# Kernel optimization log

Measured on AMD Instinct MI355X. Metric: run time of the kernel, lower is better.

Reference implementation:

```python
import jax, jax.numpy as jnp
import numpy as np

BN_EPS = 1e-5
GRID = 8  # 8x8 region grid
AU_NUM = 12


def conv2d(x, w, b, stride=1, pad=0):
    # x: [B,C,H,W], w: [O,I,kh,kw]
    y = jax.lax.conv_general_dilated(
        x, w, (stride, stride), [(pad, pad), (pad, pad)],
        dimension_numbers=("NCHW", "OIHW", "NCHW"))
    return y + b[None, :, None, None]


def bn_eval(x, gamma, beta, mean, var):
    inv = jax.lax.rsqrt(var + BN_EPS)
    return (x - mean[None, :, None, None]) * (gamma * inv)[None, :, None, None] + beta[None, :, None, None]


def region_layer(x, gamma, beta, mean, var, cw, cb):
    # x: [B,C,H,W]; per-network params indexed by k = i*j + j (faithful to source)
    B, C, H, W = x.shape
    ph, pw = H // GRID, W // GRID
    # -> [64, B, C, ph, pw]
    p = x.reshape(B, C, GRID, ph, GRID, pw).transpose(2, 4, 0, 1, 3, 5).reshape(GRID * GRID, B, C, ph, pw)
    ii = jnp.arange(GRID)[:, None]
    jj = jnp.arange(GRID)[None, :]
    idx = (ii * jj + jj).reshape(-1)  # replicates self.networks[i*j+j]

    def per_patch(xp, g, bt, m, v, w, b):
        xn = bn_eval(xp, g, bt, m, v)
        xr = jax.nn.relu(xn)
        return conv2d(xr, w, b, stride=1, pad=1) + xp

    out = jax.vmap(per_patch)(p, gamma[idx], beta[idx], mean[idx], var[idx], cw[idx], cb[idx])
    # [64,B,C,ph,pw] -> [B,C,H,W]
    return out.reshape(GRID, GRID, B, C, ph, pw).transpose(2, 3, 0, 4, 1, 5).reshape(B, C, H, W)


def maxpool2(x):
    return jax.lax.reduce_window(x, -jnp.inf, jax.lax.max, (1, 1, 2, 2), (1, 1, 2, 2), "VALID")


def setup_inputs() -> dict:
    key = jax.random.key(0)
    ks = iter(jax.random.split(key, 40))
    n = lambda shape, s=0.05: jax.random.normal(next(ks), shape, jnp.float32) * s
    d = {}
    d["x"] = jax.random.normal(next(ks), (32, 3, 170, 170), jnp.float32)
    d["conv1_w"] = n((32, 3, 11, 11)); d["conv1_b"] = n((32,))
    NG = GRID * GRID
    d["rl_gamma"] = 1.0 + n((NG, 32)); d["rl_beta"] = n((NG, 32))
    d["rl_mean"] = n((NG, 32)); d["rl_var"] = 0.5 + jax.random.uniform(next(ks), (NG, 32), jnp.float32)
    d["rl_cw"] = n((NG, 32, 32, 3, 3)); d["rl_cb"] = n((NG, 32))
    d["bn_gamma"] = 1.0 + n((32,)); d["bn_beta"] = n((32,))
    d["bn_mean"] = n((32,)); d["bn_var"] = 0.5 + jax.random.uniform(next(ks), (32,), jnp.float32)
    d["conv2_w"] = n((16, 32, 8, 8)); d["conv2_b"] = n((16,))
    d["conv3_w"] = n((16, 16, 8, 8)); d["conv3_b"] = n((16,))
    d["conv4_w"] = n((16, 16, 6, 6)); d["conv4_b"] = n((16,))
    d["conv5_w"] = n((16, 16, 5, 5)); d["conv5_b"] = n((16,))
    d["fc1_w"] = n((4096, 16 * 27 * 27), 0.01); d["fc1_b"] = n((4096,))
    d["fc2_w"] = n((2048, 4096), 0.01); d["fc2_b"] = n((2048,))
    d["fc3_w"] = n((AU_NUM * 2, 2048), 0.01); d["fc3_b"] = n((AU_NUM * 2,))
    return d


def reference(x, conv1_w, conv1_b, rl_gamma, rl_beta, rl_mean, rl_var, rl_cw, rl_cb,
              bn_gamma, bn_beta, bn_mean, bn_var, conv2_w, conv2_b, conv3_w, conv3_b,
              conv4_w, conv4_b, conv5_w, conv5_b, fc1_w, fc1_b, fc2_w, fc2_b, fc3_w, fc3_b):
    B = x.shape[0]
    h = conv2d(x, conv1_w, conv1_b)                       # [B,32,160,160]
    h = region_layer(h, rl_gamma, rl_beta, rl_mean, rl_var, rl_cw, rl_cb)
    h = jax.nn.relu(h)
    h = maxpool2(h)                                       # [B,32,80,80]
    h = bn_eval(h, bn_gamma, bn_beta, bn_mean, bn_var)
    h = jax.nn.relu(conv2d(h, conv2_w, conv2_b))          # [B,16,73,73]
    h = jax.nn.relu(conv2d(h, conv3_w, conv3_b))          # [B,16,66,66]
    h = jax.nn.relu(conv2d(h, conv4_w, conv4_b, stride=2))  # [B,16,31,31]
    h = jax.nn.relu(conv2d(h, conv5_w, conv5_b))          # [B,16,27,27]
    h = h.reshape(B, -1)
    h = jax.nn.relu(h @ fc1_w.T + fc1_b)
    h = jax.nn.relu(h @ fc2_w.T + fc2_b)  # dropout = identity (eval)
    h = h @ fc3_w.T + fc3_b
    h = h.reshape(B, 2, AU_NUM)
    return jax.nn.log_softmax(h, axis=1)
```

## Files before the change

### kernel.cpp

```cpp
#include <hip/hip_runtime.h>
#include <hip/hip_bf16.h>

typedef __hip_bfloat16 bf16;
typedef __attribute__((ext_vector_type(8))) short short8;
typedef __attribute__((ext_vector_type(4))) float f32x4;
typedef __attribute__((ext_vector_type(16))) float f32x16;

__device__ __forceinline__ float b2f(const bf16 v){ return __bfloat162float(v); }
__device__ __forceinline__ float ld(const float* p, long i){ return p[i]; }
__device__ __forceinline__ float ld(const bf16*  p, long i){ return b2f(p[i]); }

__device__ __forceinline__ unsigned f2bf_u(float f){
    union { float f; unsigned u; } a; a.f = f;
    unsigned r = a.u + 0x7FFFu + ((a.u >> 16) & 1u);
    return r >> 16;
}

__device__ __forceinline__ short8 pack8(const float* v){
    union { __hip_bfloat162 h[4]; short8 s; } r;
    #pragma unroll
    for (int i=0;i<4;i++)
        r.h[i] = __float22bfloat162_rn(float2{v[2*i], v[2*i+1]});
    return r.s;
}

__device__ __forceinline__ uint2 pack4(const float* v){
    union { __hip_bfloat162 h[2]; uint2 u; } r;
    r.h[0] = __float22bfloat162_rn(float2{v[0], v[1]});
    r.h[1] = __float22bfloat162_rn(float2{v[2], v[3]});
    return r.u;
}

__device__ __forceinline__ void unp8(uint4 u, float* v){
    union { unsigned x; float f; } a;
    a.x = u.x<<16; v[0]=a.f; a.x = u.x&0xffff0000u; v[1]=a.f;
    a.x = u.y<<16; v[2]=a.f; a.x = u.y&0xffff0000u; v[3]=a.f;
    a.x = u.z<<16; v[4]=a.f; a.x = u.z&0xffff0000u; v[5]=a.f;
    a.x = u.w<<16; v[6]=a.f; a.x = u.w&0xffff0000u; v[7]=a.f;
}

__device__ __forceinline__ void unp4(uint2 u, float* v){
    union { unsigned x; float f; } a;
    a.x = u.x<<16; v[0]=a.f; a.x = u.x&0xffff0000u; v[1]=a.f;
    a.x = u.y<<16; v[2]=a.f; a.x = u.y&0xffff0000u; v[3]=a.f;
}

#define GLD_LDS16(g, l) __builtin_amdgcn_global_load_lds( \
    (const __attribute__((address_space(1))) void*)(g), \
    (__attribute__((address_space(3))) void*)(l), 16, 0, 0)

#define OFF_C1W   0
#define OFF_C1B   11616
#define OFF_RLG   11648
#define OFF_RLB   13696
#define OFF_RLM   15744
#define OFF_RLV   17792
#define OFF_RLCW  19840
#define OFF_RLCB  609664
#define OFF_BNG   611712
#define OFF_BNB   611744
#define OFF_BNM   611776
#define OFF_BNV   611808
#define OFF_C2W   611840
#define OFF_C2B   644608
#define OFF_C3W   644624
#define OFF_C3B   661008
#define OFF_C4W   661024
#define OFF_C4B   670240
#define OFF_C5W   670256
#define OFF_C5B   676656
#define OFF_F1B   676672
#define OFF_F2B   680768
#define OFF_F3B   682816
#define P_TOTAL   682840
#define OFF_WB2   P_TOTAL
#define OFF_WB3   (P_TOTAL + 16384)
#define OFF_WC1   (P_TOTAL + 16384 + 8192)
#define P_END     (OFF_WC1 + 8448)

#define SZ_RL  589824
#define SZ_WB2 32768
#define SZ_WB3 16384
#define SZ_WC1 16896

struct CvtArgs { const void* src[23]; int off[23]; const void* cw; const void* w2; const void* w3;
                 const void* x0; int total; };

__device__ __forceinline__ float getv(const void* p, long i, bool isf){
    return isf ? ((const float*)p)[i] : b2f(((const bf16*)p)[i]);
}

__global__ __launch_bounds__(256) void k_cvt(CvtArgs a, int* __restrict__ flag,
                                             float* __restrict__ P)
{
    __shared__ int cnt;
    if (threadIdx.x == 0) cnt = 0;
    __syncthreads();
    {
        const bf16* xb = (const bf16*)a.x0;
        const float v = fabsf(b2f(xb[2*threadIdx.x]));
        if (v >= 1e-6f && v <= 1e6f) atomicAdd(&cnt, 1);
    }
    __syncthreads();
    const bool isf = (cnt < 192);
    if (blockIdx.x == 0 && threadIdx.x == 0) *flag = isf ? 1 : 0;

    const int i1 = a.total;
    const int i2 = i1 + SZ_RL;
    const int i3 = i2 + SZ_WB2;
    const int i4 = i3 + SZ_WB3;
    const int i5 = i4 + SZ_WC1;
    for (int idx = blockIdx.x*256 + threadIdx.x; idx < i5; idx += gridDim.x*256){
        if (idx < i1){
            if (idx >= OFF_RLCW && idx < OFF_RLCB) continue;
            int k = 0;
            #pragma unroll
            for (int j = 1; j < 23; j++) if (idx >= a.off[j]) k = j;
            P[idx] = getv(a.src[k], idx - a.off[k], isf);
        } else if (idx < i2){
            const int d = idx - i1;
            const int net = d / 9216, dn = d % 9216;
            const int tap = dn >> 10, rem = dn & 1023;
            const int half = rem >> 9, lane = (rem >> 3) & 63, j = rem & 7;
            const int co = half*16 + (lane & 15);
            const int ci = ((lane >> 4) << 3) + j;
            const long sidx = (long)((net*32 + co)*32 + ci)*9 + tap;
            ((unsigned short*)(P + OFF_RLCW))[d] = (unsigned short)f2bf_u(getv(a.cw, sidx, isf));
        } else if (idx < i3){
            const int d = idx - i2;
            const int j = d & 7, lane = (d >> 3) & 63, tap = d >> 9;
            const int n = lane & 15, k = ((lane >> 4) << 3) + j;
            const int ci = k, ky = tap >> 3, kx = tap & 7;
            const long sidx = (long)((n*32 + ci)*8 + ky)*8 + kx;
            ((unsigned short*)(P + OFF_WB2))[d] = (unsigned short)f2bf_u(getv(a.w2, sidx, isf));
        } else if (idx < i4){
            const int d = idx - i3;
            const int j = d & 7, lane = (d >> 3) & 63, pair = d >> 9;
            const int n = lane & 15, k = ((lane >> 4) << 3) + j;
            const int tsel = k >> 4, ci = k & 15;
            const int ky = pair >> 2, kx = ((pair & 3) << 1) + tsel;
            const long sidx = (long)((n*16 + ci)*8 + ky)*8 + kx;
            ((unsigned short*)(P + OFF_WB3))[d] = (unsigned short)f2bf_u(getv(a.w3, sidx, isf));
        } else {
            const int d = idx - i4;
            const int ky = d / 1536, rem = d % 1536;
            const int ch = rem >> 9, rem2 = rem & 511;
            const int lane = rem2 >> 3, j = rem2 & 7;
            const int co = lane & 31, h5 = lane >> 5;
            const int kx = ch*4 + h5*2 + (j >> 2), ci = j & 3;
            float v = 0.f;
            if (ci < 3 && kx < 11)
                v = getv(a.src[0], (long)((co*3 + ci)*11 + ky)*11 + kx, isf);
            ((unsigned short*)(P + OFF_WC1))[d] = (unsigned short)f2bf_u(v);
        }
    }
}

__global__ __launch_bounds__(256,3) void k_conv1M(const void* __restrict__ x,
        const int* __restrict__ flag, const float* __restrict__ P, unsigned short* __restrict__ out)
{
    __shared__ unsigned short xs[18*44*4];
    __shared__ unsigned short wsm[SZ_WC1];
    const int t = threadIdx.x;
    const int y0 = blockIdx.x*8, x0 = blockIdx.y*32, b = blockIdx.z;
    { const uint4* src = (const uint4*)(P + OFF_WC1);
      uint4* dst = (uint4*)wsm;
      for (int e=t; e<2112; e+=256) dst[e] = src[e]; }
    const bool isf = (*flag) != 0;
    for (int e=t; e<792; e+=256){
        const int r = e/44, c = e%44;
        const long base = ((long)(b*3)*170 + (y0+r))*170 + min(x0+c, 169);
        float v0, v1, v2;
        if (isf){
            const float* xf = (const float*)x;
            v0 = xf[base]; v1 = xf[base+28900]; v2 = xf[base+57800];
        } else {
            const bf16* xf = (const bf16*)x;
            v0 = b2f(xf[base]); v1 = b2f(xf[base+28900]); v2 = b2f(xf[base+57800]);
        }
        uint2 u;
        u.x = f2bf_u(v0) | (f2bf_u(v1) << 16);
        u.y = f2bf_u(v2);
        *(uint2*)&xs[(r*44+c)*4] = u;
    }
    __syncthreads();
    const int wave = t>>6, lane = t&63;
    const int n = lane & 31, h5 = lane >> 5;
    const int r0 = wave*2;
    f32x16 acc0 = {0.f}, acc1 = {0.f};
    #pragma unroll
    for (int e=0;e<16;e++){ acc0[e]=0.f; acc1[e]=0.f; }
    #pragma unroll 1
    for (int ky=0; ky<11; ky++){
        #pragma unroll
        for (int ch=0; ch<3; ch++){
            const short8 aw = *(const short8*)&wsm[((ky*3+ch)*64 + lane)*8];
            const int kx0 = ch*4 + h5*2;
            const int a0 = ((r0+ky)*44 + n + kx0)*4;
            const int a1 = ((r0+1+ky)*44 + n + kx0)*4;
            union { uint2 u2[2]; short8 s; } ub0, ub1;
            ub0.u2[0] = *(const uint2*)&xs[a0];
            ub0.u2[1] = *(const uint2*)&xs[a0+4];
            ub1.u2[0] = *(const uint2*)&xs[a1];
            ub1.u2[1] = *(const uint2*)&xs[a1+4];
            acc0 = __builtin_amdgcn_mfma_f32_32x32x16_bf16(aw, ub0.s, acc0, 0,0,0);
            acc1 = __builtin_amdgcn_mfma_f32_32x32x16_bf16(aw, ub1.s, acc1, 0,0,0);
        }
    }
    unsigned short* opb = out + ((long)b*25600 + (long)(y0+r0)*160 + x0 + n)*32;
    #pragma unroll
    for (int g=0; g<4; g++){
        const int co0 = 8*g + 4*h5;
        const f32x4 bv = *(const f32x4*)&P[OFF_C1B + co0];
        float s0[4], s1[4];
        #pragma unroll
        for (int r=0;r<4;r++){ s0[r] = acc0[4*g+r] + bv[r]; s1[r] = acc1[4*g+r] + bv[r]; }
        *(uint2*)(opb + co0) = pack4(s0);
        *(uint2*)(opb + 160*32 + co0) = pack4(s1);
    }
}

__global__ __launch_bounds__(256,2) void k_regionM(const unsigned short* __restrict__ in,
        const float* __restrict__ P, unsigned short* __restrict__ pooled)
{
    __shared__ unsigned short s_in[484*32];
    __shared__ unsigned short wsm[9216];
    __shared__ float sc[32], sh[32];
    const int t = threadIdx.x;
    const int b = blockIdx.x & 31, kk = blockIdx.x >> 5;
    const int gi = kk >> 3, gj = kk & 7;
    const int net = gj*(gi+1);
    const long pbase = ((long)b*25600 + (long)(gi*20)*160 + gj*20)*32;
    if (t < 32){
        const float inv = rsqrtf(P[OFF_RLV+net*32+t]+1e-5f)*P[OFF_RLG+net*32+t];
        sc[t] = inv; sh[t] = P[OFF_RLB+net*32+t] - P[OFF_RLM+net*32+t]*inv;
    }
    { const uint4* src = (const uint4*)((const unsigned short*)(P+OFF_RLCW) + (size_t)net*9216);
      uint4* dst = (uint4*)wsm;
      for (int e=t; e<1152; e+=256) dst[e] = src[e]; }
    __syncthreads();
    for (int e=t; e<1936; e+=256){
        const int o = e & 3, p = e >> 2;
        const int pr = p/22, pc = p%22;
        short8 pk = {0,0,0,0,0,0,0,0};
        if (pr>0 && pr<21 && pc>0 && pc<21){
            const long a = pbase + ((long)(pr-1)*160 + (pc-1))*32 + o*8;
            const uint4 u = *(const uint4*)&in[a];
            float v[8];
            unp8(u, v);
            #pragma unroll
            for (int j=0;j<8;j++){
                const int ci = o*8 + j;
                v[j] = fmaxf(fmaf(v[j], sc[ci], sh[ci]), 0.f);
            }
            pk = pack8(v);
        }
        *(short8*)&s_in[p*32 + o*8] = pk;
    }
    __syncthreads();
    const int wave = t>>6, lane = t&63;
    const int q = lane>>4, n = lane&15;
    const int dr = n>>2, dc = n&3;
    const int nt = (wave==0) ? 7 : 6;
    int trs[7], tcs[7];
    #pragma unroll
    for (int i=0;i<7;i++){ const int tt = 4*i + wave; trs[i] = tt/5; tcs[i] = tt - 5*(tt/5); }
    f32x4 acc[7][2];
    {   float bias_v[2][4];
        #pragma unroll
        for (int h=0;h<2;h++)
            #pragma unroll
            for (int r=0;r<4;r++) bias_v[h][r] = P[OFF_RLCB + net*32 + h*16 + q*4 + r];
        #pragma unroll
        for (int i=0;i<7;i++)
            #pragma unroll
            for (int h=0;h<2;h++)
                acc[i][h] = (f32x4){bias_v[h][0], bias_v[h][1], bias_v[h][2], bias_v[h][3]};
    }
    #pragma unroll 1
    for (int tap=0; tap<9; tap++){
        const short8 a0 = *(const short8*)&wsm[(tap*2+0)*512 + lane*8];
        const short8 a1 = *(const short8*)&wsm[(tap*2+1)*512 + lane*8];
        const int ky = tap/3, kx = tap - 3*(tap/3);
        #pragma unroll
        for (int i=0;i<7;i++){
            if (i < nt){
                const int srow = trs[i]*4 + dr + ky, scol = tcs[i]*4 + dc + kx;
                const short8 bx = *(const short8*)&s_in[(srow*22 + scol)*32 + q*8];
                acc[i][0] = __builtin_amdgcn_mfma_f32_16x16x32_bf16(a0, bx, acc[i][0], 0,0,0);
                acc[i][1] = __builtin_amdgcn_mfma_f32_16x16x32_bf16(a1, bx, acc[i][1], 0,0,0);
            }
        }
    }
    float bnsc[2][4], bnsh[2][4];
    #pragma unroll
    for (int h=0;h<2;h++)
        #pragma unroll
        for (int r=0;r<4;r++){
            const int co = h*16 + q*4 + r;
            const float inv = rsqrtf(P[OFF_BNV+co]+1e-5f)*P[OFF_BNG+co];
            bnsc[h][r] = inv; bnsh[h][r] = P[OFF_BNB+co] - P[OFF_BNM+co]*inv;
        }
    const bool wr = ((n & 5) == 0);
    #pragma unroll
    for (int i=0;i<7;i++){
        if (i < nt){
            const int prow = trs[i]*4 + dr, pcol = tcs[i]*4 + dc;
            const long ra = pbase + ((long)prow*160 + pcol)*32;
            const long pa0 = ((long)b*6400 + (long)(gi*10 + trs[i]*2 + (dr>>1))*80
                              + gj*10 + tcs[i]*2 + (dc>>1))*32;
            #pragma unroll
            for (int h=0;h<2;h++){
                const uint2 ru = *(const uint2*)&in[ra + h*16 + q*4];
                float res[4];
                unp4(ru, res);
                float pv[4];
                #pragma unroll
                for (int r=0;r<4;r++){
                    float v = acc[i][h][r] + res[r];
                    v = fmaxf(v, 0.f);
                    v = fmaxf(v, __shfl_xor(v, 1, 64));
                    v = fmaxf(v, __shfl_xor(v, 4, 64));
                    pv[r] = fmaf(v, bnsc[h][r], bnsh[h][r]);
                }
                if (wr) *(uint2*)&pooled[pa0 + h*16 + q*4] = pack4(pv);
            }
        }
    }
}

template<int CIN, int HIN, int WIN, int HOUT, int WOUT, bool NHWC_OUT>
__global__ __launch_bounds__(256) void k_convM(const unsigned short* __restrict__ in,
        const unsigned short* __restrict__ WB, const float* __restrict__ bias,
        void* __restrict__ outv)
{
    constexpr int PP = 23;
    constexpr bool C32 = (CIN == 32);
    __shared__ unsigned short xs[PP*PP*CIN];
    __shared__ unsigned short ws[C32 ? 16*64*8 : 32*64*8];
    const int t = threadIdx.x;
    const int col0 = blockIdx.x*16, row0 = blockIdx.y*16, b = blockIdx.z;
    for (int e = t; e < PP*PP*(CIN/8); e += 256){
        const int o = e % (CIN/8), pix = e / (CIN/8);
        int rr = row0 + pix/PP; if (rr > HIN-1) rr = HIN-1;
        int cc = col0 + pix%PP; if (cc > WIN-1) cc = WIN-1;
        const uint4 v = *(const uint4*)&in[((long)b*HIN*WIN + (long)rr*WIN + cc)*CIN + o*8];
        *(uint4*)&xs[pix*CIN + o*8] = v;
    }
    const int wave = t>>6, lane = t&63;
    const int quad = lane>>4, n16 = lane&15;
    const float bv = bias[n16];
    f32x4 acc[4];
    #pragma unroll
    for (int mt=0;mt<4;mt++) acc[mt] = (f32x4){bv,bv,bv,bv};
    if constexpr (C32){
        for (int ch=0; ch<4; ch++){
            __syncthreads();
            const unsigned* src = (const unsigned*)WB + ch*4096;
            for (int e=t; e<4096; e+=256) ((unsigned*)ws)[e] = src[e];
            __syncthreads();
            #pragma unroll 1
            for (int tap=0; tap<16; tap++){
                const int tg = ch*16+tap, ky = tg>>3, kx = tg&7;
                const short8 bw = *(const short8*)&ws[(tap*64+lane)*8];
                #pragma unroll
                for (int mt=0; mt<4; mt++){
                    const int pr = wave*4+mt+ky, pc = n16+kx;
                    const short8 av = *(const short8*)&xs[(pr*PP+pc)*32 + quad*8];
                    acc[mt] = __builtin_amdgcn_mfma_f32_16x16x32_bf16(av, bw, acc[mt], 0,0,0);
                }
            }
        }
    } else {
        for (int e=t; e<8192; e+=256) ((unsigned*)ws)[e] = ((const unsigned*)WB)[e];
        __syncthreads();
        #pragma unroll 1
        for (int pair=0; pair<32; pair++){
            const int ky = pair>>2, kx0 = (pair&3)*2;
            const short8 bw = *(const short8*)&ws[(pair*64+lane)*8];
            #pragma unroll
            for (int mt=0; mt<4; mt++){
                const int pr = wave*4+mt+ky, pc = n16 + kx0 + (quad>>1);
                const short8 av = *(const short8*)&xs[(pr*PP+pc)*16 + (quad&1)*8];
                acc[mt] = __builtin_amdgcn_mfma_f32_16x16x32_bf16(av, bw, acc[mt], 0,0,0);
            }
        }
    }
    #pragma unroll
    for (int mt=0; mt<4; mt++){
        const int orow = row0 + wave*4 + mt;
        if (orow >= HOUT) continue;
        const int ocol = col0 + quad*4;
        #pragma unroll
        for (int r=0;r<4;r++){
            if (ocol + r < WOUT){
                const float v = fmaxf(acc[mt][r], 0.f);
                if constexpr (NHWC_OUT)
                    ((unsigned short*)outv)[((long)b*HOUT*WOUT + (long)orow*WOUT + ocol + r)*16 + n16]
                        = (unsigned short)f2bf_u(v);
                else
                    ((float*)outv)[((long)(b*16 + n16)*HOUT + orow)*WOUT + ocol + r] = v;
            }
        }
    }
}

template<int CIN, int COUT, int KS, int STRIDE, int HIN, int WIN, int HOUT, int WOUT,
         int NG, int OW>
__global__ __launch_bounds__(256,2) void k_convN(const float* __restrict__ in,
        const float* __restrict__ w, const float* __restrict__ bias, float* __restrict__ out)
{
    __shared__ float wl[CIN*KS*KS];
    const int co = blockIdx.y, b = blockIdx.z;
    for (int j=threadIdx.x; j<CIN*KS*KS; j+=blockDim.x) wl[j] = w[co*CIN*KS*KS + j];
    __syncthreads();
    const int i = blockIdx.x*blockDim.x + threadIdx.x;
    if (i >= HOUT*NG) return;
    const int y = i / NG, x0 = (i % NG) * OW;
    float acc[OW];
    const float bv = bias[co];
    #pragma unroll
    for (int j=0;j<OW;j++) acc[j]=bv;
    constexpr int SPAN = STRIDE*(OW-1) + KS;
    for (int ci=0; ci<CIN; ci++){
        #pragma unroll
        for (int ky=0; ky<KS; ky++){
            const float* ip = in + ((long)(b*CIN+ci)*HIN + (STRIDE*y+ky))*WIN + STRIDE*x0;
            float v[SPAN];
            #pragma unroll
            for (int j=0;j<SPAN;j++) v[j]=ip[j];
            const float* wr = &wl[(ci*KS+ky)*KS];
            #pragma unroll
            for (int kx=0;kx<KS;kx++){
                const float wv = wr[kx];
                #pragma unroll
                for (int j=0;j<OW;j++) acc[j] = fmaf(v[STRIDE*j+kx], wv, acc[j]);
            }
        }
    }
    float* op = out + ((long)(b*COUT+co)*HOUT + y)*WOUT + x0;
    #pragma unroll
    for (int j=0;j<OW;j++)
        if (x0 + j < WOUT) op[j] = fmaxf(acc[j], 0.f);
}

__global__ __launch_bounds__(256,2) void k_conv5F(const float* __restrict__ in,
        const float* __restrict__ P, unsigned short* __restrict__ xp, float* __restrict__ y)
{
    __shared__ float wl[16*25];
    const int co = blockIdx.y, b = blockIdx.z;
    const int t = threadIdx.x;
    for (int j=t; j<400; j+=256) wl[j] = P[OFF_C5W + co*400 + j];
    {   const int lin = (b*16 + co)*256 + t;
        y[lin] = P[OFF_F1B + (lin & 4095)];
    }
    if (co == 0 && t < 208){
        unsigned short* pp = xp + (long)b*12288 + 11664 + t*3;
        pp[0] = 0; pp[1] = 0; pp[2] = 0;
    }
    __syncthreads();
    if (t >= 27*7) return;
    const int yy = t / 7, x0 = (t % 7) * 4;
    float acc[4];
    const float bv = P[OFF_C5B + co];
    #pragma unroll
    for (int j=0;j<4;j++) acc[j]=bv;
    for (int ci=0; ci<16; ci++){
        #pragma unroll
        for (int ky=0; ky<5; ky++){
            const float* ip = in + ((long)(b*16+ci)*31 + (yy+ky))*31 + x0;
            float v[8];
            #pragma unroll
            for (int j=0;j<8;j++) v[j]=ip[j];
            const float* wr = &wl[(ci*5+ky)*5];
            #pragma unroll
            for (int kx=0;kx<5;kx++){
                const float wv = wr[kx];
                #pragma unroll
                for (int j=0;j<4;j++) acc[j] = fmaf(v[j+kx], wv, acc[j]);
            }
        }
    }
    unsigned short* op = xp + (long)b*12288 + (co*27 + yy)*27 + x0;
    #pragma unroll
    for (int j=0;j<4;j++)
        if (x0 + j < 27) op[j] = (unsigned short)f2bf_u(fmaxf(acc[j], 0.f));
}

__global__ __launch_bounds__(256) void k_pk(const float* __restrict__ in,
        unsigned short* __restrict__ out, float* __restrict__ y,
        const float* __restrict__ bias, int N, int ny, int rows, int K)
{
    const int i = blockIdx.x*256 + threadIdx.x;
    if (i < ny){ y[i] = bias[i % N]; return; }
    const int d = i - ny;
    const int per = K >> 3;
    if (d >= rows*per) return;
    const int row = d / per, k = (d - row*per)*8;
    float v[8];
    *(f32x4*)&v[0] = *(const f32x4*)&in[(long)row*K + k];
    *(f32x4*)&v[4] = *(const f32x4*)&in[(long)row*K + k + 4];
    #pragma unroll
    for (int j=0;j<8;j++) v[j] = fmaxf(v[j], 0.f);
    *(short8*)&out[(long)row*K + k] = pack8(v);
}

template<typename WT>
__device__ __forceinline__ void fcl_body(const unsigned short* __restrict__ x,
        const WT* __restrict__ w, float* __restrict__ y,
        int Kw, int Khat, int N, int Kc, int Nvalid, unsigned char* lbuf)
{
    constexpr bool WF = __is_same(WT, float);
    const int t = threadIdx.x;
    const int wave = t>>6, lane = t&63;
    const int quad = lane>>4, n16 = lane&15;
    const int og = wave>>1, bh = wave&1;
    const int bx = blockIdx.x;
    const int start = blockIdx.y*Kc;
    int steps = 0;
    {   const int rem = Kw - start;
        const int sa = Kc >> 7;
        if (rem > 0){ steps = (rem + 127) >> 7; if (steps > sa) steps = sa; }
    }
    f32x4 acc = {0.f,0.f,0.f,0.f};
    const unsigned short* xp = x + (long)(bh*16 + n16)*Khat;
    const int row = og*16 + n16;

    auto stage = [&](int s, int bsel){
        const int k0 = start + (s<<7);
        const bool swz = (k0 + 128 <= Kw);
        unsigned char* base = lbuf + bsel*16384;
        if constexpr (WF){
            const int r0 = wave*8;
            #pragma unroll
            for (int c=0;c<4;c++){
                const int rr = r0 + 2*c + (lane>>5);
                const int cs = swz ? ((lane&31) ^ (rr&7)) : (lane&31);
                long koff = (long)k0 + cs*4;
                const float* ga = w + (long)(bx*32 + rr)*Kw + koff;
                if (!swz && (koff + 4 > Kw)) ga = w + (long)(bx*32 + rr)*Kw;
                GLD_LDS16(ga, base + (r0 + 2*c)*512);
            }
        } else {
            const int r0 = wave*8;
            #pragma unroll
            for (int c=0;c<2;c++){
                const int rr = r0 + 4*c + (lane>>4);
                const int cs = swz ? ((lane&15) ^ (rr&7)) : (lane&15);
                long koff = (long)k0 + cs*8;
                const WT* ga = w + (long)(bx*32 + rr)*Kw + koff;
                if (!swz && (koff + 8 > Kw)) ga = w + (long)(bx*32 + rr)*Kw;
                GLD_LDS16(ga, base + (r0 + 4*c)*256);
            }
        }
    };
    auto consume = [&](int s, int bsel){
        const int k0 = start + (s<<7);
        const bool swz = (k0 + 128 <= Kw);
        const unsigned char* base = lbuf + bsel*16384;
        #pragma unroll
        for (int kk=0; kk<4; kk++){
            const int ka = k0 + kk*32 + quad*8;
            const short8 x8 = *(const short8*)&xp[ka];
            short8 bw;
            if constexpr (WF){
                const int c0 = kk*8 + quad*2;
                const int p0 = swz ? (c0 ^ (row&7)) : c0;
                const int p1 = swz ? ((c0+1) ^ (row&7)) : (c0+1);
                float wv[8];
                *(f32x4*)&wv[0] = *(const f32x4*)&base[row*512 + p0*16];
                *(f32x4*)&wv[4] = *(const f32x4*)&base[row*512 + p1*16];
                bw = pack8(wv);
            } else {
                const int c0 = kk*4 + quad;
                const int p0 = swz ? (c0 ^ (row&7)) : c0;
                bw = *(const short8*)&base[row*256 + p0*16];
            }
            acc = __builtin_amdgcn_mfma_f32_16x16x32_bf16(x8, bw, acc, 0,0,0);
        }
    };

    if (steps > 0){
        stage(0, 0);
        __syncthreads();
        for (int s=0; s<steps; s++){
            if (s+1 < steps) stage(s+1, (s+1)&1);
            consume(s, s&1);
            __syncthreads();
        }
    }
    const int o = bx*32 + og*16 + n16;
    if (o < Nvalid){
        #pragma unroll
        for (int r=0;r<4;r++)
            atomicAdd(&y[(long)(bh*16 + quad*4 + r)*N + o], acc[r]);
    }
}

__global__ __launch_bounds__(256,4) void k_fcL(const unsigned short* __restrict__ x,
        const void* __restrict__ w, const int* __restrict__ flag,
        float* __restrict__ y, int Kw, int Khat, int N, int Kc, int Nvalid)
{
    __shared__ unsigned char lbuf[2*16384];
    if (*flag) fcl_body<float>(x, (const float*)w, y, Kw, Khat, N, Kc, Nvalid, lbuf);
    else       fcl_body<bf16 >(x, (const bf16 *)w, y, Kw, Khat, N, Kc, Nvalid, lbuf);
}

template<typename WT>
__device__ __forceinline__ void fcm_loop(const unsigned short* __restrict__ xp,
        const WT* __restrict__ wp, int start, int end, int quad, f32x4& acc)
{
    const int nfull = (end - start) >> 5;
    const int end32 = start + (nfull << 5);
    const int qo = quad*8;

    short8 xA, xB, xC;
    short8 bwA, bwB, bwC;
    f32x4 wA0, wA1, wB0, wB1, wC0, wC1;

    auto loadA = [&](int k0){
        const int ka = k0 + qo;
        xA = *(const short8*)&xp[ka];
        if constexpr (__is_same(WT, bf16)) bwA = *(const short8*)&wp[ka];
        else { wA0 = *(const f32x4*)&wp[ka]; wA1 = *(const f32x4*)&wp[ka+4]; }
    };
    auto loadB = [&](int k0){
        const int ka = k0 + qo;
        xB = *(const short8*)&xp[ka];
        if constexpr (__is_same(WT, bf16)) bwB = *(const short8*)&wp[ka];
        else { wB0 = *(const f32x4*)&wp[ka]; wB1 = *(const f32x4*)&wp[ka+4]; }
    };
    auto loadC = [&](int k0){
        const int ka = k0 + qo;
        xC = *(const short8*)&xp[ka];
        if constexpr (__is_same(WT, bf16)) bwC = *(const short8*)&wp[ka];
        else { wC0 = *(const f32x4*)&wp[ka]; wC1 = *(const f32x4*)&wp[ka+4]; }
    };
    auto compA = [&](){
        short8 bw;
        if constexpr (__is_same(WT, bf16)) bw = bwA;
        else { float wv[8]; *(f32x4*)&wv[0]=wA0; *(f32x4*)&wv[4]=wA1; bw = pack8(wv); }
        acc = __builtin_amdgcn_mfma_f32_16x16x32_bf16(xA, bw, acc, 0,0,0);
    };
    auto compB = [&](){
        short8 bw;
        if constexpr (__is_same(WT, bf16)) bw = bwB;
        else { float wv[8]; *(f32x4*)&wv[0]=wB0; *(f32x4*)&wv[4]=wB1; bw = pack8(wv); }
        acc = __builtin_amdgcn_mfma_f32_16x16x32_bf16(xB, bw, acc, 0,0,0);
    };
    auto compC = [&](){
        short8 bw;
        if constexpr (__is_same(WT, bf16)) bw = bwC;
        else { float wv[8]; *(f32x4*)&wv[0]=wC0; *(f32x4*)&wv[4]=wC1; bw = pack8(wv); }
        acc = __builtin_amdgcn_mfma_f32_16x16x32_bf16(xC, bw, acc, 0,0,0);
    };

    if (nfull >= 3){
        loadA(start); loadB(start+32); loadC(start+64);
        int j = 0;
        for (; j + 6 <= nfull; j += 3){
            compA(); loadA(start + ((j+3)<<5));
            compB(); loadB(start + ((j+4)<<5));
            compC(); loadC(start + ((j+5)<<5));
        }
        const int rem = nfull - j;
        if (rem == 3){ compA(); compB(); compC(); }
        else if (rem == 4){
            compA(); loadA(start + ((j+3)<<5));
            compB(); compC(); compA();
        } else {
            compA(); loadA(start + ((j+3)<<5));
            compB(); loadB(start + ((j+4)<<5));
            compC(); compA(); compB();
        }
    } else if (nfull == 2){
        loadA(start); loadB(start+32); compA(); compB();
    } else if (nfull == 1){
        loadA(start); compA();
    }
    if (end32 < end){
        const int ka = end32 + qo;
        float xv[8], wv[8];
        #pragma unroll
        for (int j=0;j<8;j++){
            const bool v = (ka + j) < end;
            xv[j] = v ? b2f(((const bf16*)xp)[ka+j]) : 0.f;
            wv[j] = v ? (float)ld(wp, ka+j) : 0.f;
        }
        acc = __builtin_amdgcn_mfma_f32_16x16x32_bf16(pack8(xv), pack8(wv), acc, 0,0,0);
    }
}

__global__ __launch_bounds__(256,4) void k_fcM(const unsigned short* __restrict__ x,
        const void* __restrict__ w, const int* __restrict__ flag,
        float* __restrict__ y, int K, int N, int Kc, int Nvalid)
{
    const int t = threadIdx.x;
    const int wave = t>>6, lane = t&63;
    const int quad = lane>>4, n16 = lane&15;
    const int og = wave>>1, bh = wave&1;
    const int o = blockIdx.x*32 + og*16 + n16;
    const int orow = (o < Nvalid) ? o : (Nvalid-1);
    const int xrow = bh*16 + n16;
    const int start = blockIdx.y*Kc;
    const int end = min(K, start + Kc);
    f32x4 acc = {0.f,0.f,0.f,0.f};
    const unsigned short* xp = x + (long)xrow*K;
    if (*flag) fcm_loop<float>(xp, (const float*)w + (long)orow*K, start, end, quad, acc);
    else       fcm_loop<bf16 >(xp, (const bf16 *)w + (long)orow*K, start, end, quad, acc);
    if (o < Nvalid){
        #pragma unroll
        for (int r=0;r<4;r++)
            atomicAdd(&y[(long)(bh*16 + quad*4 + r)*N + o], acc[r]);
    }
}

__global__ void k_lsm(const float* __restrict__ in, const int* __restrict__ flag,
                      void* __restrict__ out)
{
    const int i = threadIdx.x;
    if (i >= 384) return;
    const int b = i/12, au = i%12;
    const float a0 = in[b*24+au], a1 = in[b*24+12+au];
    const float m = fmaxf(a0,a1);
    const float lse = m + logf(expf(a0-m)+expf(a1-m));
    const float o0 = a0-lse, o1 = a1-lse;
    if (*flag){
        ((float*)out)[b*24+au]    = o0;
        ((float*)out)[b*24+12+au] = o1;
    } else {
        ((bf16*)out)[b*24+au]    = __float2bfloat16(o0);
        ((bf16*)out)[b*24+12+au] = __float2bfloat16(o1);
    }
}

extern "C" void kernel_launch(void* const* d_in, const int* in_sizes, int n_in,
                              void* d_out, int out_size, void* d_ws, size_t ws_size,
                              hipStream_t stream) {
    (void)in_sizes; (void)n_in; (void)out_size; (void)ws_size;
    const void* x = d_in[0];

    float* A = (float*)d_ws;
    float* B = A + 26214400;
    float* P = B + 6553600;
    int* flag = (int*)(P + P_END);
    unsigned short* Xp = (unsigned short*)(P + P_END + 16);
    unsigned short* Abf = (unsigned short*)A;
    unsigned short* Bbf = (unsigned short*)B;
    float* Bhi = B + 5000000;

    CvtArgs a;
    const int src_idx[23] = {1,2,3,4,5,6,7,8,9,10,11,12,13,14,15,16,17,18,19,20,22,24,26};
    const int offs[23] = {OFF_C1W,OFF_C1B,OFF_RLG,OFF_RLB,OFF_RLM,OFF_RLV,OFF_RLCW,OFF_RLCB,
                          OFF_BNG,OFF_BNB,OFF_BNM,OFF_BNV,OFF_C2W,OFF_C2B,OFF_C3W,OFF_C3B,
                          OFF_C4W,OFF_C4B,OFF_C5W,OFF_C5B,OFF_F1B,OFF_F2B,OFF_F3B};
    for (int j=0;j<23;j++){ a.src[j] = d_in[src_idx[j]]; a.off[j] = offs[j]; }
    a.cw = d_in[7]; a.w2 = d_in[13]; a.w3 = d_in[15];
    a.x0 = x;
    a.total = P_TOTAL;

    k_cvt<<<(P_TOTAL+SZ_RL+SZ_WB2+SZ_WB3+SZ_WC1+255)/256,256,0,stream>>>(a, flag, P);
    k_conv1M<<<dim3(20,5,32),256,0,stream>>>(x, flag, P, Abf);
    k_regionM<<<2048,256,0,stream>>>(Abf, P, Bbf);
    k_convM<32,80,80,73,73,true><<<dim3(5,5,32),256,0,stream>>>(Bbf, (const unsigned short*)(P+OFF_WB2), P+OFF_C2B, (void*)Abf);
    k_convM<16,73,73,66,66,false><<<dim3(5,5,32),256,0,stream>>>(Abf, (const unsigned short*)(P+OFF_WB3), P+OFF_C3B, (void*)B);
    k_convN<16,16,6,2,66,66,31,31,8,4><<<dim3(1,16,32),256,0,stream>>>(B, P+OFF_C4W, P+OFF_C4B, Bhi);
    k_conv5F<<<dim3(1,16,32),256,0,stream>>>(Bhi, P, Xp, A);
    k_fcL<<<dim3(128,8),256,0,stream>>>(Xp, d_in[21], flag, A, 11664, 12288, 4096, 1536, 4096);
    k_pk<<<(65536+16384+255)/256,256,0,stream>>>(A, Xp, B, P+OFF_F2B, 2048, 65536, 32, 4096);
    k_fcL<<<dim3(64,8),256,0,stream>>>(Xp, d_in[23], flag, B, 4096, 4096, 2048, 512, 2048);
    k_pk<<<(768+8192+255)/256,256,0,stream>>>(B, Xp, A, P+OFF_F3B, 24, 768, 32, 2048);
    k_fcM<<<dim3(1,64),256,0,stream>>>(Xp, d_in[25], flag, A, 2048, 24, 32, 24);
    k_lsm<<<1,384,0,stream>>>(A, flag, d_out);
}
```

Before: 569.7 us.

## Enlarge conv1 row tile, retile conv4 over channel pairs, skip cvt hole

Three separate changes. In conv1, each wave now computes four output rows instead of two, which halves the number of blocks and amortises the per-block weight staging into shared memory; the cost is more accumulator registers and the occupancy hint dropping from 3 to 2. Conv4 is rewritten so each block handles two output channels and 16 rows with all 256 threads active, where before only 248 of 256 were busy in a single-channel block. The conversion kernel compacts its index space so threads no longer iterate over and skip the region-conv weight hole.

```diff
diff --git a/kernel.cpp b/kernel.cpp
--- a/kernel.cpp
+++ b/kernel.cpp
@@ -82,6 +82,7 @@
 #define SZ_WB2 32768
 #define SZ_WB3 16384
 #define SZ_WC1 16896
+#define SZ_HOLE (OFF_RLCB - OFF_RLCW)
 
 struct CvtArgs { const void* src[23]; int off[23]; const void* cw; const void* w2; const void* w3;
                  const void* x0; int total; };
@@ -105,20 +106,20 @@
     const bool isf = (cnt < 192);
     if (blockIdx.x == 0 && threadIdx.x == 0) *flag = isf ? 1 : 0;
 
-    const int i1 = a.total;
-    const int i2 = i1 + SZ_RL;
-    const int i3 = i2 + SZ_WB2;
-    const int i4 = i3 + SZ_WB3;
-    const int i5 = i4 + SZ_WC1;
-    for (int idx = blockIdx.x*256 + threadIdx.x; idx < i5; idx += gridDim.x*256){
-        if (idx < i1){
-            if (idx >= OFF_RLCW && idx < OFF_RLCB) continue;
+    const int c1 = P_TOTAL - SZ_HOLE;
+    const int c2 = c1 + SZ_RL;
+    const int c3 = c2 + SZ_WB2;
+    const int c4 = c3 + SZ_WB3;
+    const int c5 = c4 + SZ_WC1;
+    for (int c = blockIdx.x*256 + threadIdx.x; c < c5; c += gridDim.x*256){
+        if (c < c1){
+            const int idx = (c < OFF_RLCW) ? c : (c + SZ_HOLE);
             int k = 0;
             #pragma unroll
             for (int j = 1; j < 23; j++) if (idx >= a.off[j]) k = j;
             P[idx] = getv(a.src[k], idx - a.off[k], isf);
-        } else if (idx < i2){
-            const int d = idx - i1;
+        } else if (c < c2){
+            const int d = c - c1;
             const int net = d / 9216, dn = d % 9216;
             const int tap = dn >> 10, rem = dn & 1023;
             const int half = rem >> 9, lane = (rem >> 3) & 63, j = rem & 7;
@@ -126,15 +127,15 @@
             const int ci = ((lane >> 4) << 3) + j;
             const long sidx = (long)((net*32 + co)*32 + ci)*9 + tap;
             ((unsigned short*)(P + OFF_RLCW))[d] = (unsigned short)f2bf_u(getv(a.cw, sidx, isf));
-        } else if (idx < i3){
-            const int d = idx - i2;
+        } else if (c < c3){
+            const int d = c - c2;
             const int j = d & 7, lane = (d >> 3) & 63, tap = d >> 9;
             const int n = lane & 15, k = ((lane >> 4) << 3) + j;
             const int ci = k, ky = tap >> 3, kx = tap & 7;
             const long sidx = (long)((n*32 + ci)*8 + ky)*8 + kx;
             ((unsigned short*)(P + OFF_WB2))[d] = (unsigned short)f2bf_u(getv(a.w2, sidx, isf));
-        } else if (idx < i4){
-            const int d = idx - i3;
+        } else if (c < c4){
+            const int d = c - c3;
             const int j = d & 7, lane = (d >> 3) & 63, pair = d >> 9;
             const int n = lane & 15, k = ((lane >> 4) << 3) + j;
             const int tsel = k >> 4, ci = k & 15;
@@ -142,7 +143,7 @@
             const long sidx = (long)((n*16 + ci)*8 + ky)*8 + kx;
             ((unsigned short*)(P + OFF_WB3))[d] = (unsigned short)f2bf_u(getv(a.w3, sidx, isf));
         } else {
-            const int d = idx - i4;
+            const int d = c - c4;
             const int ky = d / 1536, rem = d % 1536;
             const int ch = rem >> 9, rem2 = rem & 511;
             const int lane = rem2 >> 3, j = rem2 & 7;
@@ -156,18 +157,18 @@
     }
 }
 
-__global__ __launch_bounds__(256,3) void k_conv1M(const void* __restrict__ x,
+__global__ __launch_bounds__(256,2) void k_conv1M(const void* __restrict__ x,
         const int* __restrict__ flag, const float* __restrict__ P, unsigned short* __restrict__ out)
 {
-    __shared__ unsigned short xs[18*44*4];
+    __shared__ unsigned short xs[26*44*4];
     __shared__ unsigned short wsm[SZ_WC1];
     const int t = threadIdx.x;
-    const int y0 = blockIdx.x*8, x0 = blockIdx.y*32, b = blockIdx.z;
+    const int y0 = blockIdx.x*16, x0 = blockIdx.y*32, b = blockIdx.z;
     { const uint4* src = (const uint4*)(P + OFF_WC1);
       uint4* dst = (uint4*)wsm;
       for (int e=t; e<2112; e+=256) dst[e] = src[e]; }
     const bool isf = (*flag) != 0;
-    for (int e=t; e<792; e+=256){
+    for (int e=t; e<1144; e+=256){
         const int r = e/44, c = e%44;
         const long base = ((long)(b*3)*170 + (y0+r))*170 + min(x0+c, 169);
         float v0, v1, v2;
@@ -186,37 +187,45 @@
     __syncthreads();
     const int wave = t>>6, lane = t&63;
     const int n = lane & 31, h5 = lane >> 5;
-    const int r0 = wave*2;
-    f32x16 acc0 = {0.f}, acc1 = {0.f};
-    #pragma unroll
-    for (int e=0;e<16;e++){ acc0[e]=0.f; acc1[e]=0.f; }
+    const int r0 = wave*4;
+    f32x16 acc0 = {0.f}, acc1 = {0.f}, acc2 = {0.f}, acc3 = {0.f};
+    #pragma unroll
+    for (int e=0;e<16;e++){ acc0[e]=0.f; acc1[e]=0.f; acc2[e]=0.f; acc3[e]=0.f; }
     #pragma unroll 1
     for (int ky=0; ky<11; ky++){
         #pragma unroll
         for (int ch=0; ch<3; ch++){
             const short8 aw = *(const short8*)&wsm[((ky*3+ch)*64 + lane)*8];
             const int kx0 = ch*4 + h5*2;
-            const int a0 = ((r0+ky)*44 + n + kx0)*4;
-            const int a1 = ((r0+1+ky)*44 + n + kx0)*4;
-            union { uint2 u2[2]; short8 s; } ub0, ub1;
-            ub0.u2[0] = *(const uint2*)&xs[a0];
-            ub0.u2[1] = *(const uint2*)&xs[a0+4];
-            ub1.u2[0] = *(const uint2*)&xs[a1];
-            ub1.u2[1] = *(const uint2*)&xs[a1+4];
+            const int ab = ((r0+ky)*44 + n + kx0)*4;
+            union { uint2 u2[2]; short8 s; } ub0, ub1, ub2, ub3;
+            ub0.u2[0] = *(const uint2*)&xs[ab];
+            ub0.u2[1] = *(const uint2*)&xs[ab+4];
+            ub1.u2[0] = *(const uint2*)&xs[ab+176];
+            ub1.u2[1] = *(const uint2*)&xs[ab+180];
+            ub2.u2[0] = *(const uint2*)&xs[ab+352];
+            ub2.u2[1] = *(const uint2*)&xs[ab+356];
+            ub3.u2[0] = *(const uint2*)&xs[ab+528];
+            ub3.u2[1] = *(const uint2*)&xs[ab+532];
             acc0 = __builtin_amdgcn_mfma_f32_32x32x16_bf16(aw, ub0.s, acc0, 0,0,0);
             acc1 = __builtin_amdgcn_mfma_f32_32x32x16_bf16(aw, ub1.s, acc1, 0,0,0);
-        }
-    }
-    unsigned short* opb = out + ((long)b*25600 + (long)(y0+r0)*160 + x0 + n)*32;
-    #pragma unroll
-    for (int g=0; g<4; g++){
-        const int co0 = 8*g + 4*h5;
-        const f32x4 bv = *(const f32x4*)&P[OFF_C1B + co0];
-        float s0[4], s1[4];
-        #pragma unroll
-        for (int r=0;r<4;r++){ s0[r] = acc0[4*g+r] + bv[r]; s1[r] = acc1[4*g+r] + bv[r]; }
-        *(uint2*)(opb + co0) = pack4(s0);
-        *(uint2*)(opb + 160*32 + co0) = pack4(s1);
+            acc2 = __builtin_amdgcn_mfma_f32_32x32x16_bf16(aw, ub2.s, acc2, 0,0,0);
+            acc3 = __builtin_amdgcn_mfma_f32_32x32x16_bf16(aw, ub3.s, acc3, 0,0,0);
+        }
+    }
+    #pragma unroll
+    for (int s=0; s<4; s++){
+        unsigned short* opb = out + ((long)b*25600 + (long)(y0+r0+s)*160 + x0 + n)*32;
+        const f32x16* ap = (s==0) ? &acc0 : (s==1) ? &acc1 : (s==2) ? &acc2 : &acc3;
+        #pragma unroll
+        for (int g=0; g<4; g++){
+            const int co0 = 8*g + 4*h5;
+            const f32x4 bv = *(const f32x4*)&P[OFF_C1B + co0];
+            float sv[4];
+            #pragma unroll
+            for (int r=0;r<4;r++) sv[r] = (*ap)[4*g+r] + bv[r];
+            *(uint2*)(opb + co0) = pack4(sv);
+        }
     }
 }
 
@@ -405,43 +414,46 @@
     }
 }
 
-template<int CIN, int COUT, int KS, int STRIDE, int HIN, int WIN, int HOUT, int WOUT,
-         int NG, int OW>
-__global__ __launch_bounds__(256,2) void k_convN(const float* __restrict__ in,
-        const float* __restrict__ w, const float* __restrict__ bias, float* __restrict__ out)
-{
-    __shared__ float wl[CIN*KS*KS];
-    const int co = blockIdx.y, b = blockIdx.z;
-    for (int j=threadIdx.x; j<CIN*KS*KS; j+=blockDim.x) wl[j] = w[co*CIN*KS*KS + j];
+__global__ __launch_bounds__(256,2) void k_conv4(const float* __restrict__ in,
+        const float* __restrict__ P, float* __restrict__ out)
+{
+    __shared__ float wl[2*16*36];
+    const int cp = blockIdx.y, bx = blockIdx.x, b = blockIdx.z;
+    const int t = threadIdx.x;
+    for (int j=t; j<1152; j+=256) wl[j] = P[OFF_C4W + cp*1152 + j];
     __syncthreads();
-    const int i = blockIdx.x*blockDim.x + threadIdx.x;
-    if (i >= HOUT*NG) return;
-    const int y = i / NG, x0 = (i % NG) * OW;
-    float acc[OW];
-    const float bv = bias[co];
-    #pragma unroll
-    for (int j=0;j<OW;j++) acc[j]=bv;
-    constexpr int SPAN = STRIDE*(OW-1) + KS;
-    for (int ci=0; ci<CIN; ci++){
-        #pragma unroll
-        for (int ky=0; ky<KS; ky++){
-            const float* ip = in + ((long)(b*CIN+ci)*HIN + (STRIDE*y+ky))*WIN + STRIDE*x0;
-            float v[SPAN];
-            #pragma unroll
-            for (int j=0;j<SPAN;j++) v[j]=ip[j];
-            const float* wr = &wl[(ci*KS+ky)*KS];
-            #pragma unroll
-            for (int kx=0;kx<KS;kx++){
+    const int cl = t>>7;
+    const int rem = t&127;
+    const int r = bx*16 + (rem>>3);
+    const int grp = rem&7;
+    const int x0 = grp*4;
+    if (r >= 31) return;
+    const int co = cp*2 + cl;
+    float acc[4];
+    const float bv = P[OFF_C4B + co];
+    #pragma unroll
+    for (int j=0;j<4;j++) acc[j]=bv;
+    const float* wc = &wl[cl*576];
+    for (int ci=0; ci<16; ci++){
+        #pragma unroll
+        for (int ky=0; ky<6; ky++){
+            const float* ip = in + ((long)(b*16+ci)*66 + (2*r+ky))*66 + 2*x0;
+            float v[12];
+            #pragma unroll
+            for (int j=0;j<12;j++) v[j]=ip[j];
+            const float* wr = &wc[(ci*6+ky)*6];
+            #pragma unroll
+            for (int kx=0;kx<6;kx++){
                 const float wv = wr[kx];
                 #pragma unroll
-                for (int j=0;j<OW;j++) acc[j] = fmaf(v[STRIDE*j+kx], wv, acc[j]);
-            }
-        }
-    }
-    float* op = out + ((long)(b*COUT+co)*HOUT + y)*WOUT + x0;
-    #pragma unroll
-    for (int j=0;j<OW;j++)
-        if (x0 + j < WOUT) op[j] = fmaxf(acc[j], 0.f);
+                for (int j=0;j<4;j++) acc[j] = fmaf(v[2*j+kx], wv, acc[j]);
+            }
+        }
+    }
+    float* op = out + ((long)(b*16+co)*31 + r)*31 + x0;
+    #pragma unroll
+    for (int j=0;j<4;j++)
+        if (x0 + j < 31) op[j] = fmaxf(acc[j], 0.f);
 }
 
 __global__ __launch_bounds__(256,2) void k_conv5F(const float* __restrict__ in,
@@ -759,12 +771,12 @@
     a.x0 = x;
     a.total = P_TOTAL;
 
-    k_cvt<<<(P_TOTAL+SZ_RL+SZ_WB2+SZ_WB3+SZ_WC1+255)/256,256,0,stream>>>(a, flag, P);
-    k_conv1M<<<dim3(20,5,32),256,0,stream>>>(x, flag, P, Abf);
+    k_cvt<<<((P_TOTAL-SZ_HOLE)+SZ_RL+SZ_WB2+SZ_WB3+SZ_WC1+255)/256,256,0,stream>>>(a, flag, P);
+    k_conv1M<<<dim3(10,5,32),256,0,stream>>>(x, flag, P, Abf);
     k_regionM<<<2048,256,0,stream>>>(Abf, P, Bbf);
     k_convM<32,80,80,73,73,true><<<dim3(5,5,32),256,0,stream>>>(Bbf, (const unsigned short*)(P+OFF_WB2), P+OFF_C2B, (void*)Abf);
     k_convM<16,73,73,66,66,false><<<dim3(5,5,32),256,0,stream>>>(Abf, (const unsigned short*)(P+OFF_WB3), P+OFF_C3B, (void*)B);
-    k_convN<16,16,6,2,66,66,31,31,8,4><<<dim3(1,16,32),256,0,stream>>>(B, P+OFF_C4W, P+OFF_C4B, Bhi);
+    k_conv4<<<dim3(2,8,32),256,0,stream>>>(B, P, Bhi);
     k_conv5F<<<dim3(1,16,32),256,0,stream>>>(Bhi, P, Xp, A);
     k_fcL<<<dim3(128,8),256,0,stream>>>(Xp, d_in[21], flag, A, 11664, 12288, 4096, 1536, 4096);
     k_pk<<<(65536+16384+255)/256,256,0,stream>>>(A, Xp, B, P+OFF_F2B, 2048, 65536, 32, 4096);
```

New measurement: 557.4 us. 2.2% less time.
